# Kernel tuning notes

Hardware: AMD Instinct MI355X
Metric: run time of the kernel (lower is better)

The kernel has to match this reference:

```python
import jax, jax.numpy as jnp
import numpy as np
import math

MAX_SIZE = 2048  # max_size init arg


def setup_inputs() -> dict:
    key = jax.random.key(0)
    k1, k2, k3 = jax.random.split(key, 3)
    B, S, D = 16, 1024, 512
    PRED = 256
    data = jax.random.normal(k1, (B, S, D), dtype=jnp.float32)
    W = jax.random.normal(k2, (PRED, D), dtype=jnp.float32) * (1.0 / math.sqrt(D))
    b = jax.random.normal(k3, (PRED,), dtype=jnp.float32) * 0.01
    return {"data": data, "W": W, "b": b}


def reference(data, W, b):
    # data: [B, S, D]; self-attention with q=k=v=data
    B, S, D = data.shape
    pred_len = W.shape[0]
    scale = 1.0 / math.sqrt(D)
    scores = jnp.einsum('bsd,btd->bst', data, data) * scale          # [B,S,S]
    prob = jax.nn.softmax(scores, axis=-1)
    attn = jnp.einsum('bst,btd->bsd', prob, data)                     # [B,S,D]
    # NOTE: the original concatenates a 'mask' block (rows S..2S) onto attn,
    # but the per-timestep Linear loop only reads rows 0..S-1, so the mask
    # never affects the output (dead code). The loop collapses to one GEMM.
    lin = jnp.einsum('bsd,pd->bsp', attn, W) + b                      # [B,S,pred_len]
    out = jnp.zeros((B, MAX_SIZE, pred_len), dtype=data.dtype)
    out = out.at[:, :S, :].set(lin)
    return out
```

## Files before the change

kernel.cpp:

```cpp
#include <hip/hip_runtime.h>
#include <cstdint>
#include <cstddef>

#define B_    16
#define S_    1024
#define D_    512
#define P_    256
#define MAXS_ 2048

typedef unsigned short u16;
typedef unsigned int   u32;
typedef _Float16 f16;
typedef _Float16 f16x8 __attribute__((ext_vector_type(8)));
typedef float  f32x4  __attribute__((ext_vector_type(4)));
typedef unsigned short u16x4 __attribute__((ext_vector_type(4)));
typedef unsigned short u16x8 __attribute__((ext_vector_type(8)));

__device__ __forceinline__ void gld_lds16(const void* g, void* l) {
  __builtin_amdgcn_global_load_lds(
      (const __attribute__((address_space(1))) u32*)g,
      (__attribute__((address_space(3))) u32*)l, 16, 0, 0);
}

__device__ __forceinline__ u16 f2h(float f) {
  return __builtin_bit_cast(u16, (f16)f);
}
__device__ __forceinline__ float h2f(u16 h) {
  return (float)__builtin_bit_cast(f16, h);
}

template<int N> __device__ __forceinline__ void waitvm() {
  if constexpr (N == 0)       asm volatile("s_waitcnt vmcnt(0)" ::: "memory");
  else if constexpr (N == 8)  asm volatile("s_waitcnt vmcnt(8)" ::: "memory");
  else if constexpr (N == 20) asm volatile("s_waitcnt vmcnt(20)" ::: "memory");
  else static_assert(N != N, "unsupported vmcnt literal");
}

__global__ void convert_f16_kernel(const float* __restrict__ src, u16* __restrict__ dst, long n4) {
  long stride = (long)gridDim.x * blockDim.x;
  for (long i = (long)blockIdx.x * blockDim.x + threadIdx.x; i < n4; i += stride) {
    float4 v = ((const float4*)src)[i];
    u16x4 o;
    o[0] = f2h(v.x); o[1] = f2h(v.y); o[2] = f2h(v.z); o[3] = f2h(v.w);
    ((u16x4*)dst)[i] = o;
  }
}

template<int EPI, int KK, int BM, int BN, int NW, int WNS, int MINW>
__global__ __launch_bounds__(NW * 64, MINW) void gemm_pipe(
    const u16* __restrict__ A, const u16* __restrict__ Bm,
    void* __restrict__ C, const float* __restrict__ bias,
    long sAb, long sBb, long sCb, int LDC, float scale) {
  constexpr int T   = NW * 64;
  constexpr int WMS = NW / WNS;
  constexpr int MF  = BM / (WMS * 16);
  constexpr int NF  = BN / (WNS * 16);
  constexpr int LA  = BM * 8 / T;
  constexpr int LB  = BN * 8 / T;
  constexpr int L   = LA + LB;
  constexpr int SZ  = (BM + BN) * 128;
  constexpr int NT  = KK / 64;
  static_assert(MF * NF == 32, "wave tile must be 32 frags");

  extern __shared__ __align__(16) char smem[];

  const int tid  = threadIdx.x;
  const int lane = tid & 63;
  const int w    = tid >> 6;
  const int wm   = w / WNS;
  const int wn   = w % WNS;
  const int lr   = lane & 15;
  const int hi   = lane >> 4;

  const int bz = blockIdx.z;
  const int I0 = blockIdx.y * BM;
  const int J0 = blockIdx.x * BN;

  if constexpr (EPI == 2) {
    if (I0 >= S_) {
      float4* o = (float4*)C + ((long)bz * sCb + (size_t)I0 * LDC) / 4;
      const int n4 = BM * LDC / 4;
      for (int i = tid; i < n4; i += T) o[i] = make_float4(0.f, 0.f, 0.f, 0.f);
      return;
    }
  }

  const u16* Ab = A  + (long)bz * sAb;
  const u16* Bb = Bm + (long)bz * sBb;

  auto stage = [&](int buf, int k0) {
    char* sA = smem + buf * SZ;
    char* sB = sA + BM * 128;
    #pragma unroll
    for (int i = 0; i < LA; ++i) {
      int cid = i * T + tid;
      int row = cid >> 3;
      int c   = (cid & 7) ^ (row & 7);
      gld_lds16(Ab + (size_t)(I0 + row) * KK + k0 + c * 8, sA + cid * 16);
    }
    #pragma unroll
    for (int i = 0; i < LB; ++i) {
      int cid = i * T + tid;
      int row = cid >> 3;
      int c   = (cid & 7) ^ (row & 7);
      gld_lds16(Bb + (size_t)(J0 + row) * KK + k0 + c * 8, sB + cid * 16);
    }
  };

  f32x4 acc[MF][NF] = {};

  stage(0, 0);
  for (int t = 0; t < NT; ++t) {
    const char* lA = smem + (t & 1) * SZ;
    const char* lB = lA + BM * 128;

    if (t + 1 < NT) { stage((t + 1) & 1, (t + 1) * 64); waitvm<L>(); }
    else            { waitvm<0>(); }
    __builtin_amdgcn_s_barrier();
    __builtin_amdgcn_sched_barrier(0);

    #pragma unroll
    for (int kk = 0; kk < 2; ++kk) {
      f16x8 af[MF], bf[NF];
      #pragma unroll
      for (int m = 0; m < MF; ++m) {
        int row = wm * (MF * 16) + m * 16 + lr;
        int cp  = (kk * 4 + hi) ^ (row & 7);
        af[m] = *(const f16x8*)(lA + ((row * 8 + cp) << 4));
      }
      #pragma unroll
      for (int n = 0; n < NF; ++n) {
        int row = wn * (NF * 16) + n * 16 + lr;
        int cp  = (kk * 4 + hi) ^ (row & 7);
        bf[n] = *(const f16x8*)(lB + ((row * 8 + cp) << 4));
      }
      __builtin_amdgcn_s_setprio(1);
      #pragma unroll
      for (int m = 0; m < MF; ++m)
        #pragma unroll
        for (int n = 0; n < NF; ++n)
          acc[m][n] = __builtin_amdgcn_mfma_f32_16x16x32_f16(af[m], bf[n], acc[m][n], 0, 0, 0);
      __builtin_amdgcn_s_setprio(0);
    }
    __builtin_amdgcn_sched_barrier(0);
    __builtin_amdgcn_s_barrier();
  }

  const int row0 = I0 + wm * (MF * 16);
  const int col0 = J0 + wn * (NF * 16);
  float bv[NF];
  if constexpr (EPI == 2) {
    #pragma unroll
    for (int n = 0; n < NF; ++n) bv[n] = bias[col0 + n * 16 + lr];
  }
  #pragma unroll
  for (int m = 0; m < MF; ++m) {
    #pragma unroll
    for (int i = 0; i < 4; ++i) {
      int r = row0 + m * 16 + (hi << 2) + i;
      #pragma unroll
      for (int n = 0; n < NF; ++n) {
        int c = col0 + n * 16 + lr;
        float v = acc[m][n][i];
        long off = (long)bz * sCb + (size_t)r * LDC + c;
        if constexpr (EPI == 0) {
          ((u16*)C)[off] = f2h(v * scale);
        } else if constexpr (EPI == 1) {
          ((u16*)C)[off] = f2h(v);
        } else {
          ((float*)C)[off] = v + bv[n];
        }
      }
    }
  }
}

__global__ __launch_bounds__(256) void softmax_kernel(
    const u16* __restrict__ scores, u16* __restrict__ prob) {
  const int lane = threadIdx.x & 63;
  const int wv   = threadIdx.x >> 6;
  const long row = (long)blockIdx.x * 4 + wv;
  const u16* src = scores + row * S_;

  u16x8 a0 = *(const u16x8*)&src[lane * 16];
  u16x8 a1 = *(const u16x8*)&src[lane * 16 + 8];
  float v[16];
  #pragma unroll
  for (int j = 0; j < 8; ++j) { v[j] = h2f(a0[j]); v[8 + j] = h2f(a1[j]); }

  float mx = -3.4e38f;
  #pragma unroll
  for (int j = 0; j < 16; ++j) mx = fmaxf(mx, v[j]);
  #pragma unroll
  for (int off = 32; off > 0; off >>= 1)
    mx = fmaxf(mx, __shfl_xor(mx, off));

  const float l2e = 1.4426950408889634f;
  float sum = 0.f;
  #pragma unroll
  for (int j = 0; j < 16; ++j) { v[j] = exp2f((v[j] - mx) * l2e); sum += v[j]; }
  #pragma unroll
  for (int off = 32; off > 0; off >>= 1)
    sum += __shfl_xor(sum, off);
  const float inv = 1.f / sum;

  u16x8 o0, o1;
  #pragma unroll
  for (int j = 0; j < 8; ++j) { o0[j] = f2h(v[j] * inv); o1[j] = f2h(v[8 + j] * inv); }
  *(u16x8*)&prob[row * S_ + lane * 16]     = o0;
  *(u16x8*)&prob[row * S_ + lane * 16 + 8] = o1;
}

extern "C" void kernel_launch(void* const* d_in, const int* in_sizes, int n_in,
                              void* d_out, int out_size, void* d_ws, size_t ws_size,
                              hipStream_t stream) {
  const float* data = (const float*)d_in[0];
  const float* W    = (const float*)d_in[1];
  const float* bias = (const float*)d_in[2];
  float* out = (float*)d_out;
  char*  ws  = (char*)d_ws;

  const size_t MB = 1024 * 1024;
  u16* dataH  = (u16*)(ws);
  u16* Wh     = (u16*)(ws + 16 * MB);
  u16* scoresH= (u16*)(ws + 17 * MB);
  u16* probH  = (u16*)(ws + 49 * MB);
  u16* VWT    = (u16*)(ws + 81 * MB);

  const float scale = 0.04419417382415922f;

  constexpr int SMEM_BIG  = 2 * (256 + 256) * 128;
  constexpr int SMEM_WIDE = 2 * (64 + 256) * 128;

  auto* kG1 = (const void*)&gemm_pipe<0, 512,  256, 256, 8, 4, 2>;
  auto* kVW = (const void*)&gemm_pipe<1, 512,  64,  256, 2, 2, 1>;
  auto* kG2 = (const void*)&gemm_pipe<2, 1024, 64,  256, 2, 2, 1>;
  hipFuncSetAttribute(kG1, hipFuncAttributeMaxDynamicSharedMemorySize, SMEM_BIG);
  hipFuncSetAttribute(kVW, hipFuncAttributeMaxDynamicSharedMemorySize, SMEM_WIDE);
  hipFuncSetAttribute(kG2, hipFuncAttributeMaxDynamicSharedMemorySize, SMEM_WIDE);

  convert_f16_kernel<<<2048, 256, 0, stream>>>(data, dataH, (long)B_ * S_ * D_ / 4);
  convert_f16_kernel<<<64, 256, 0, stream>>>(W, Wh, (long)P_ * D_ / 4);

  gemm_pipe<1, 512, 64, 256, 2, 2, 1><<<dim3(4, 4, 16), 128, SMEM_WIDE, stream>>>(
      Wh, dataH, (void*)VWT, nullptr,
      0L, (long)S_ * D_, (long)P_ * S_, S_, 0.f);

  gemm_pipe<0, 512, 256, 256, 8, 4, 2><<<dim3(4, 4, 16), 512, SMEM_BIG, stream>>>(
      dataH, dataH, (void*)scoresH, nullptr,
      (long)S_ * D_, (long)S_ * D_, (long)S_ * S_, S_, scale);

  softmax_kernel<<<4096, 256, 0, stream>>>(scoresH, probH);

  gemm_pipe<2, 1024, 64, 256, 2, 2, 1><<<dim3(1, 32, 16), 128, SMEM_WIDE, stream>>>(
      probH, VWT, (void*)out, bias,
      (long)S_ * S_, (long)P_ * S_, (long)MAXS_ * P_, P_, 0.f);
}
```

Baseline: 92.70 us.

## Fuse softmax into prob·VW GEMM and deepen QK^T pipeline

```diff
diff --git a/kernel.cpp b/kernel.cpp
--- a/kernel.cpp
+++ b/kernel.cpp
@@ -29,13 +29,6 @@
   return (float)__builtin_bit_cast(f16, h);
 }
 
-template<int N> __device__ __forceinline__ void waitvm() {
-  if constexpr (N == 0)       asm volatile("s_waitcnt vmcnt(0)" ::: "memory");
-  else if constexpr (N == 8)  asm volatile("s_waitcnt vmcnt(8)" ::: "memory");
-  else if constexpr (N == 20) asm volatile("s_waitcnt vmcnt(20)" ::: "memory");
-  else static_assert(N != N, "unsupported vmcnt literal");
-}
-
 __global__ void convert_f16_kernel(const float* __restrict__ src, u16* __restrict__ dst, long n4) {
   long stride = (long)gridDim.x * blockDim.x;
   for (long i = (long)blockIdx.x * blockDim.x + threadIdx.x; i < n4; i += stride) {
@@ -46,24 +39,284 @@
   }
 }
 
-template<int EPI, int KK, int BM, int BN, int NW, int WNS, int MINW>
-__global__ __launch_bounds__(NW * 64, MINW) void gemm_pipe(
+__global__ __launch_bounds__(512, 2) void qk_pipe(
+    const u16* __restrict__ A, u16* __restrict__ Cout, float scale) {
+  extern __shared__ __align__(16) char smem[];
+  const int tid  = threadIdx.x;
+  const int lane = tid & 63;
+  const int w    = tid >> 6;
+  const int wm   = w >> 2;
+  const int wn   = w & 3;
+  const int lr   = lane & 15;
+  const int hi   = lane >> 4;
+
+  const int bz = blockIdx.z;
+  const int I0 = blockIdx.y * 256;
+  const int J0 = blockIdx.x * 256;
+  const u16* Ab = A + (long)bz * (S_ * D_);
+
+  auto stageP = [&](int s, int part) {
+    if (s >= 16) return;
+    char* dst = smem + (s & 3) * 32768 + part * 16384;
+    const int base = part ? J0 : I0;
+    const int k0 = s * 32;
+    #pragma unroll
+    for (int i = 0; i < 2; ++i) {
+      int cid   = i * 512 + tid;
+      int inner = cid >> 2;
+      int c     = (cid & 3) ^ ((inner >> 1) & 3);
+      gld_lds16(Ab + (size_t)(base + inner) * D_ + k0 + c * 8, dst + cid * 16);
+    }
+  };
+
+  f32x4 acc[8][4] = {};
+
+  stageP(0, 0); stageP(0, 1);
+  stageP(1, 0); stageP(1, 1);
+  stageP(2, 0); stageP(2, 1);
+  asm volatile("s_waitcnt vmcnt(8)" ::: "memory");
+  __builtin_amdgcn_s_barrier();
+
+  for (int s = 0; s < 16; ++s) {
+    const char* sl = smem + (s & 3) * 32768;
+    f16x8 bf[4];
+    {
+      f16x8 af[4];
+      #pragma unroll
+      for (int mq = 0; mq < 4; ++mq) {
+        int row = wm * 128 + mq * 16 + lr;
+        int cp  = hi ^ ((row >> 1) & 3);
+        af[mq] = *(const f16x8*)(sl + row * 64 + cp * 16);
+      }
+      #pragma unroll
+      for (int n = 0; n < 4; ++n) {
+        int row = wn * 64 + n * 16 + lr;
+        int cp  = hi ^ ((row >> 1) & 3);
+        bf[n] = *(const f16x8*)(sl + 16384 + row * 64 + cp * 16);
+      }
+      stageP(s + 3, 0);
+      __builtin_amdgcn_s_barrier();
+      asm volatile("s_waitcnt lgkmcnt(0)" ::: "memory");
+      __builtin_amdgcn_sched_barrier(0);
+      __builtin_amdgcn_s_setprio(1);
+      #pragma unroll
+      for (int mq = 0; mq < 4; ++mq)
+        #pragma unroll
+        for (int n = 0; n < 4; ++n)
+          acc[mq][n] = __builtin_amdgcn_mfma_f32_16x16x32_f16(af[mq], bf[n], acc[mq][n], 0, 0, 0);
+      __builtin_amdgcn_s_setprio(0);
+      __builtin_amdgcn_s_barrier();
+    }
+    {
+      f16x8 af[4];
+      #pragma unroll
+      for (int mq = 0; mq < 4; ++mq) {
+        int row = wm * 128 + 64 + mq * 16 + lr;
+        int cp  = hi ^ ((row >> 1) & 3);
+        af[mq] = *(const f16x8*)(sl + row * 64 + cp * 16);
+      }
+      stageP(s + 3, 1);
+      __builtin_amdgcn_s_barrier();
+      asm volatile("s_waitcnt lgkmcnt(0)" ::: "memory");
+      __builtin_amdgcn_sched_barrier(0);
+      __builtin_amdgcn_s_setprio(1);
+      #pragma unroll
+      for (int mq = 0; mq < 4; ++mq)
+        #pragma unroll
+        for (int n = 0; n < 4; ++n)
+          acc[4 + mq][n] = __builtin_amdgcn_mfma_f32_16x16x32_f16(af[mq], bf[n], acc[4 + mq][n], 0, 0, 0);
+      __builtin_amdgcn_s_setprio(0);
+      if (s <= 12)      asm volatile("s_waitcnt vmcnt(8)" ::: "memory");
+      else if (s == 13) asm volatile("s_waitcnt vmcnt(4)" ::: "memory");
+      else if (s == 14) asm volatile("s_waitcnt vmcnt(0)" ::: "memory");
+      __builtin_amdgcn_s_barrier();
+    }
+  }
+
+  u16* Cb = Cout + (long)bz * S_ * S_;
+  const int row0 = I0 + wm * 128;
+  const int col0 = J0 + wn * 64;
+  #pragma unroll
+  for (int m = 0; m < 8; ++m) {
+    #pragma unroll
+    for (int i = 0; i < 4; ++i) {
+      int r = row0 + m * 16 + (hi << 2) + i;
+      #pragma unroll
+      for (int n = 0; n < 4; ++n) {
+        int c = col0 + n * 16 + lr;
+        Cb[(size_t)r * S_ + c] = f2h(acc[m][n][i] * scale);
+      }
+    }
+  }
+}
+
+__global__ __launch_bounds__(512, 4) void smpv_kernel(
+    const u16* __restrict__ scores, const u16* __restrict__ VWT,
+    float* __restrict__ out, const float* __restrict__ bias) {
+  extern __shared__ __align__(16) char smem[];
+  constexpr int SZB = 8192 + 32768;
+  const int tid  = threadIdx.x;
+  const int lane = tid & 63;
+  const int w    = tid >> 6;
+  const int bz   = blockIdx.z;
+  const int yt   = blockIdx.y;
+
+  float* ob = out + (long)bz * MAXS_ * P_;
+  if (yt >= 16) {
+    float4* o = (float4*)(ob + (size_t)yt * 64 * P_);
+    for (int i = tid; i < 64 * P_ / 4; i += 512)
+      o[i] = make_float4(0.f, 0.f, 0.f, 0.f);
+    return;
+  }
+
+  const int q0 = yt * 64;
+  const u16* sb = scores + ((long)bz * S_ + q0) * S_;
+  const float l2e = 1.4426950408889634f;
+
+  float* smStat = (float*)smem;
+  {
+    const u16* rp = sb + (size_t)(w * 8) * S_ + lane * 16;
+    for (int j = 0; j < 8; ++j) {
+      u16x8 a0 = *(const u16x8*)(rp + (size_t)j * S_);
+      u16x8 a1 = *(const u16x8*)(rp + (size_t)j * S_ + 8);
+      float v[16];
+      #pragma unroll
+      for (int k = 0; k < 8; ++k) { v[k] = h2f(a0[k]); v[8 + k] = h2f(a1[k]); }
+      float mx = v[0];
+      #pragma unroll
+      for (int k = 1; k < 16; ++k) mx = fmaxf(mx, v[k]);
+      #pragma unroll
+      for (int off = 32; off > 0; off >>= 1) mx = fmaxf(mx, __shfl_xor(mx, off));
+      float sum = 0.f;
+      #pragma unroll
+      for (int k = 0; k < 16; ++k) sum += exp2f((v[k] - mx) * l2e);
+      #pragma unroll
+      for (int off = 32; off > 0; off >>= 1) sum += __shfl_xor(sum, off);
+      if (lane == 0) {
+        smStat[(w * 8 + j) * 2]     = mx;
+        smStat[(w * 8 + j) * 2 + 1] = 1.f / sum;
+      }
+    }
+  }
+  __syncthreads();
+  const int   arow = tid >> 3;
+  const float am   = smStat[arow * 2];
+  const float ail  = smStat[arow * 2 + 1];
+  __syncthreads();
+
+  const int wm = w >> 2, wn = w & 3;
+  const u16* Vb = VWT + (long)bz * P_ * S_;
+  const int ac8 = tid & 7;
+
+  auto stageB = [&](int buf, int k0) {
+    char* dB = smem + buf * SZB + 8192;
+    #pragma unroll
+    for (int i = 0; i < 4; ++i) {
+      int cid = i * 512 + tid;
+      int row = cid >> 3;
+      int c   = (cid & 7) ^ (row & 7);
+      gld_lds16(Vb + (size_t)row * S_ + k0 + c * 8, dB + cid * 16);
+    }
+  };
+  auto writeA = [&](int buf, u16x8 raw) {
+    u16x8 pv;
+    #pragma unroll
+    for (int j = 0; j < 8; ++j)
+      pv[j] = f2h(exp2f((h2f(raw[j]) - am) * l2e) * ail);
+    int c = ac8 ^ (arow & 7);
+    *(u16x8*)(smem + buf * SZB + (arow * 8 + c) * 16) = pv;
+  };
+
+  f32x4 acc[2][4] = {};
+
+  {
+    u16x8 a0 = *(const u16x8*)(sb + (size_t)arow * S_ + ac8 * 8);
+    __builtin_amdgcn_sched_barrier(0);
+    stageB(0, 0);
+    __builtin_amdgcn_sched_barrier(0);
+    asm volatile("s_waitcnt vmcnt(4)" ::: "memory");
+    writeA(0, a0);
+    asm volatile("s_waitcnt vmcnt(0) lgkmcnt(0)" ::: "memory");
+    __builtin_amdgcn_s_barrier();
+  }
+
+  for (int t = 0; t < 16; ++t) {
+    const int cur = t & 1;
+    const char* lA = smem + cur * SZB;
+    const char* lB = lA + 8192;
+
+    u16x8 anx;
+    if (t < 15) {
+      anx = *(const u16x8*)(sb + (size_t)arow * S_ + (t + 1) * 64 + ac8 * 8);
+      __builtin_amdgcn_sched_barrier(0);
+      stageB(cur ^ 1, (t + 1) * 64);
+      __builtin_amdgcn_sched_barrier(0);
+    }
+
+    #pragma unroll
+    for (int kk = 0; kk < 2; ++kk) {
+      f16x8 af[2], bfv[4];
+      #pragma unroll
+      for (int m = 0; m < 2; ++m) {
+        int row = wm * 32 + m * 16 + (lane & 15);
+        int cp  = (kk * 4 + (lane >> 4)) ^ (row & 7);
+        af[m] = *(const f16x8*)(lA + ((row * 8 + cp) << 4));
+      }
+      #pragma unroll
+      for (int n = 0; n < 4; ++n) {
+        int row = wn * 64 + n * 16 + (lane & 15);
+        int cp  = (kk * 4 + (lane >> 4)) ^ (row & 7);
+        bfv[n] = *(const f16x8*)(lB + ((row * 8 + cp) << 4));
+      }
+      __builtin_amdgcn_s_setprio(1);
+      #pragma unroll
+      for (int m = 0; m < 2; ++m)
+        #pragma unroll
+        for (int n = 0; n < 4; ++n)
+          acc[m][n] = __builtin_amdgcn_mfma_f32_16x16x32_f16(af[m], bfv[n], acc[m][n], 0, 0, 0);
+      __builtin_amdgcn_s_setprio(0);
+    }
+
+    if (t < 15) {
+      asm volatile("s_waitcnt vmcnt(4)" ::: "memory");
+      writeA(cur ^ 1, anx);
+      asm volatile("s_waitcnt vmcnt(0) lgkmcnt(0)" ::: "memory");
+      __builtin_amdgcn_s_barrier();
+    }
+  }
+
+  const int lr = lane & 15, hi = lane >> 4;
+  const int row0 = q0 + wm * 32;
+  const int col0 = wn * 64;
+  float bv[4];
+  #pragma unroll
+  for (int n = 0; n < 4; ++n) bv[n] = bias[col0 + n * 16 + lr];
+  #pragma unroll
+  for (int m = 0; m < 2; ++m) {
+    #pragma unroll
+    for (int i = 0; i < 4; ++i) {
+      int r = row0 + m * 16 + (hi << 2) + i;
+      #pragma unroll
+      for (int n = 0; n < 4; ++n)
+        ob[(size_t)r * P_ + col0 + n * 16 + lr] = acc[m][n][i] + bv[n];
+    }
+  }
+}
+
+template<int KK, int BM, int BN, int NW, int WNS>
+__global__ __launch_bounds__(NW * 64, 1) void gemm_nt_small(
     const u16* __restrict__ A, const u16* __restrict__ Bm,
-    void* __restrict__ C, const float* __restrict__ bias,
-    long sAb, long sBb, long sCb, int LDC, float scale) {
+    u16* __restrict__ C, long sAb, long sBb, long sCb, int LDC) {
   constexpr int T   = NW * 64;
   constexpr int WMS = NW / WNS;
   constexpr int MF  = BM / (WMS * 16);
   constexpr int NF  = BN / (WNS * 16);
   constexpr int LA  = BM * 8 / T;
   constexpr int LB  = BN * 8 / T;
-  constexpr int L   = LA + LB;
   constexpr int SZ  = (BM + BN) * 128;
   constexpr int NT  = KK / 64;
-  static_assert(MF * NF == 32, "wave tile must be 32 frags");
 
   extern __shared__ __align__(16) char smem[];
-
   const int tid  = threadIdx.x;
   const int lane = tid & 63;
   const int w    = tid >> 6;
@@ -75,16 +328,6 @@
   const int bz = blockIdx.z;
   const int I0 = blockIdx.y * BM;
   const int J0 = blockIdx.x * BN;
-
-  if constexpr (EPI == 2) {
-    if (I0 >= S_) {
-      float4* o = (float4*)C + ((long)bz * sCb + (size_t)I0 * LDC) / 4;
-      const int n4 = BM * LDC / 4;
-      for (int i = tid; i < n4; i += T) o[i] = make_float4(0.f, 0.f, 0.f, 0.f);
-      return;
-    }
-  }
-
   const u16* Ab = A  + (long)bz * sAb;
   const u16* Bb = Bm + (long)bz * sBb;
 
@@ -108,20 +351,21 @@
   };
 
   f32x4 acc[MF][NF] = {};
-
   stage(0, 0);
   for (int t = 0; t < NT; ++t) {
     const char* lA = smem + (t & 1) * SZ;
     const char* lB = lA + BM * 128;
-
-    if (t + 1 < NT) { stage((t + 1) & 1, (t + 1) * 64); waitvm<L>(); }
-    else            { waitvm<0>(); }
+    if (t + 1 < NT) {
+      stage((t + 1) & 1, (t + 1) * 64);
+      asm volatile("s_waitcnt vmcnt(%0)" :: "i"(LA + LB) : "memory");
+    } else {
+      asm volatile("s_waitcnt vmcnt(0)" ::: "memory");
+    }
     __builtin_amdgcn_s_barrier();
     __builtin_amdgcn_sched_barrier(0);
-
     #pragma unroll
     for (int kk = 0; kk < 2; ++kk) {
-      f16x8 af[MF], bf[NF];
+      f16x8 af[MF], bfv[NF];
       #pragma unroll
       for (int m = 0; m < MF; ++m) {
         int row = wm * (MF * 16) + m * 16 + lr;
@@ -132,14 +376,14 @@
       for (int n = 0; n < NF; ++n) {
         int row = wn * (NF * 16) + n * 16 + lr;
         int cp  = (kk * 4 + hi) ^ (row & 7);
-        bf[n] = *(const f16x8*)(lB + ((row * 8 + cp) << 4));
+        bfv[n] = *(const f16x8*)(lB + ((row * 8 + cp) << 4));
       }
       __builtin_amdgcn_s_setprio(1);
       #pragma unroll
       for (int m = 0; m < MF; ++m)
         #pragma unroll
         for (int n = 0; n < NF; ++n)
-          acc[m][n] = __builtin_amdgcn_mfma_f32_16x16x32_f16(af[m], bf[n], acc[m][n], 0, 0, 0);
+          acc[m][n] = __builtin_amdgcn_mfma_f32_16x16x32_f16(af[m], bfv[n], acc[m][n], 0, 0, 0);
       __builtin_amdgcn_s_setprio(0);
     }
     __builtin_amdgcn_sched_barrier(0);
@@ -148,67 +392,15 @@
 
   const int row0 = I0 + wm * (MF * 16);
   const int col0 = J0 + wn * (NF * 16);
-  float bv[NF];
-  if constexpr (EPI == 2) {
-    #pragma unroll
-    for (int n = 0; n < NF; ++n) bv[n] = bias[col0 + n * 16 + lr];
-  }
   #pragma unroll
-  for (int m = 0; m < MF; ++m) {
+  for (int m = 0; m < MF; ++m)
     #pragma unroll
     for (int i = 0; i < 4; ++i) {
       int r = row0 + m * 16 + (hi << 2) + i;
       #pragma unroll
-      for (int n = 0; n < NF; ++n) {
-        int c = col0 + n * 16 + lr;
-        float v = acc[m][n][i];
-        long off = (long)bz * sCb + (size_t)r * LDC + c;
-        if constexpr (EPI == 0) {
-          ((u16*)C)[off] = f2h(v * scale);
-        } else if constexpr (EPI == 1) {
-          ((u16*)C)[off] = f2h(v);
-        } else {
-          ((float*)C)[off] = v + bv[n];
-        }
-      }
-    }
-  }
-}
-
-__global__ __launch_bounds__(256) void softmax_kernel(
-    const u16* __restrict__ scores, u16* __restrict__ prob) {
-  const int lane = threadIdx.x & 63;
-  const int wv   = threadIdx.x >> 6;
-  const long row = (long)blockIdx.x * 4 + wv;
-  const u16* src = scores + row * S_;
-
-  u16x8 a0 = *(const u16x8*)&src[lane * 16];
-  u16x8 a1 = *(const u16x8*)&src[lane * 16 + 8];
-  float v[16];
-  #pragma unroll
-  for (int j = 0; j < 8; ++j) { v[j] = h2f(a0[j]); v[8 + j] = h2f(a1[j]); }
-
-  float mx = -3.4e38f;
-  #pragma unroll
-  for (int j = 0; j < 16; ++j) mx = fmaxf(mx, v[j]);
-  #pragma unroll
-  for (int off = 32; off > 0; off >>= 1)
-    mx = fmaxf(mx, __shfl_xor(mx, off));
-
-  const float l2e = 1.4426950408889634f;
-  float sum = 0.f;
-  #pragma unroll
-  for (int j = 0; j < 16; ++j) { v[j] = exp2f((v[j] - mx) * l2e); sum += v[j]; }
-  #pragma unroll
-  for (int off = 32; off > 0; off >>= 1)
-    sum += __shfl_xor(sum, off);
-  const float inv = 1.f / sum;
-
-  u16x8 o0, o1;
-  #pragma unroll
-  for (int j = 0; j < 8; ++j) { o0[j] = f2h(v[j] * inv); o1[j] = f2h(v[8 + j] * inv); }
-  *(u16x8*)&prob[row * S_ + lane * 16]     = o0;
-  *(u16x8*)&prob[row * S_ + lane * 16 + 8] = o1;
+      for (int n = 0; n < NF; ++n)
+        C[(long)bz * sCb + (size_t)r * LDC + col0 + n * 16 + lr] = f2h(acc[m][n][i]);
+    }
 }
 
 extern "C" void kernel_launch(void* const* d_in, const int* in_sizes, int n_in,
@@ -221,38 +413,32 @@
   char*  ws  = (char*)d_ws;
 
   const size_t MB = 1024 * 1024;
-  u16* dataH  = (u16*)(ws);
-  u16* Wh     = (u16*)(ws + 16 * MB);
-  u16* scoresH= (u16*)(ws + 17 * MB);
-  u16* probH  = (u16*)(ws + 49 * MB);
-  u16* VWT    = (u16*)(ws + 81 * MB);
+  u16* dataH   = (u16*)(ws);
+  u16* Wh      = (u16*)(ws + 16 * MB);
+  u16* scoresH = (u16*)(ws + 17 * MB);
+  u16* VWT     = (u16*)(ws + 49 * MB);
 
   const float scale = 0.04419417382415922f;
 
-  constexpr int SMEM_BIG  = 2 * (256 + 256) * 128;
-  constexpr int SMEM_WIDE = 2 * (64 + 256) * 128;
-
-  auto* kG1 = (const void*)&gemm_pipe<0, 512,  256, 256, 8, 4, 2>;
-  auto* kVW = (const void*)&gemm_pipe<1, 512,  64,  256, 2, 2, 1>;
-  auto* kG2 = (const void*)&gemm_pipe<2, 1024, 64,  256, 2, 2, 1>;
-  hipFuncSetAttribute(kG1, hipFuncAttributeMaxDynamicSharedMemorySize, SMEM_BIG);
-  hipFuncSetAttribute(kVW, hipFuncAttributeMaxDynamicSharedMemorySize, SMEM_WIDE);
-  hipFuncSetAttribute(kG2, hipFuncAttributeMaxDynamicSharedMemorySize, SMEM_WIDE);
+  constexpr int SMEM_QK   = 4 * 32768;
+  constexpr int SMEM_SMPV = 2 * (8192 + 32768);
+  constexpr int SMEM_VW   = 2 * (64 + 256) * 128;
+
+  (void)hipFuncSetAttribute((const void*)&qk_pipe,
+                      hipFuncAttributeMaxDynamicSharedMemorySize, SMEM_QK);
+  (void)hipFuncSetAttribute((const void*)&smpv_kernel,
+                      hipFuncAttributeMaxDynamicSharedMemorySize, SMEM_SMPV);
+  (void)hipFuncSetAttribute((const void*)&gemm_nt_small<512, 64, 256, 2, 2>,
+                      hipFuncAttributeMaxDynamicSharedMemorySize, SMEM_VW);
 
   convert_f16_kernel<<<2048, 256, 0, stream>>>(data, dataH, (long)B_ * S_ * D_ / 4);
   convert_f16_kernel<<<64, 256, 0, stream>>>(W, Wh, (long)P_ * D_ / 4);
 
-  gemm_pipe<1, 512, 64, 256, 2, 2, 1><<<dim3(4, 4, 16), 128, SMEM_WIDE, stream>>>(
-      Wh, dataH, (void*)VWT, nullptr,
-      0L, (long)S_ * D_, (long)P_ * S_, S_, 0.f);
-
-  gemm_pipe<0, 512, 256, 256, 8, 4, 2><<<dim3(4, 4, 16), 512, SMEM_BIG, stream>>>(
-      dataH, dataH, (void*)scoresH, nullptr,
-      (long)S_ * D_, (long)S_ * D_, (long)S_ * S_, S_, scale);
-
-  softmax_kernel<<<4096, 256, 0, stream>>>(scoresH, probH);
-
-  gemm_pipe<2, 1024, 64, 256, 2, 2, 1><<<dim3(1, 32, 16), 128, SMEM_WIDE, stream>>>(
-      probH, VWT, (void*)out, bias,
-      (long)S_ * S_, (long)P_ * S_, (long)MAXS_ * P_, P_, 0.f);
-}
+  gemm_nt_small<512, 64, 256, 2, 2><<<dim3(4, 4, 16), 128, SMEM_VW, stream>>>(
+      Wh, dataH, VWT, 0L, (long)S_ * D_, (long)P_ * S_, S_);
+
+  qk_pipe<<<dim3(4, 4, 16), 512, SMEM_QK, stream>>>(dataH, scoresH, scale);
+
+  smpv_kernel<<<dim3(1, 32, 16), 512, SMEM_SMPV, stream>>>(
+      scoresH, VWT, out, bias);
+}
```

New measurement: 94.29 us. Within noise of the previous version (+1.7%).
